# Performance work log

Hardware: AMD Instinct MI355X
Metric: run time of the kernel (lower is better)

Reference implementation:

```python
import jax, jax.numpy as jnp
import numpy as np

N_NODES = 100000
N_EDGES = 1600000
F_IN = 128
D = 2           # stalk dimension (2D rotations)
H = 16          # hidden channels per stalk dim
GH = 64         # gnn hidden of sheaf learner
N_LAYERS = 2
OUT = 10


def setup_inputs() -> dict:
    key = jax.random.key(0)
    ks = jax.random.split(key, 16)
    def w(k, shape):
        fan_in = shape[-2] if len(shape) >= 2 else shape[-1]
        return jax.random.normal(k, shape, dtype=jnp.float32) / jnp.sqrt(jnp.float32(fan_in))
    return {
        "x": jax.random.normal(ks[0], (N_NODES, F_IN), dtype=jnp.float32),
        "edge_index": jax.random.randint(ks[1], (2, N_EDGES), 0, N_NODES, dtype=jnp.int64),
        "W_in": w(ks[2], (F_IN, D * H)),
        "b_in": jnp.zeros((D * H,), jnp.float32),
        "emb1_W": w(ks[3], (D * H, GH)),
        "emb1_b": jnp.zeros((GH,), jnp.float32),
        "Ws1": w(ks[4], (GH, GH)),
        "Wn1": w(ks[5], (GH, GH)),
        "Ws2": w(ks[6], (GH, GH)),
        "Wn2": w(ks[7], (GH, GH)),
        "emb2_W": w(ks[8], (GH, 1)),
        "emb2_b": jnp.zeros((1,), jnp.float32),
        "W_diff": w(ks[9], (N_LAYERS, H, H)),
        "W_out": w(ks[10], (D * H, OUT)),
        "b_out": jnp.zeros((OUT,), jnp.float32),
    }


def reference(x, edge_index, W_in, b_in, emb1_W, emb1_b, Ws1, Wn1, Ws2, Wn2,
              emb2_W, emb2_b, W_diff, W_out, b_out):
    src, dst = edge_index[0], edge_index[1]
    n = x.shape[0]

    # input embedding to node stalk features
    h = x @ W_in + b_in                               # (N, D*H)

    m = jax.nn.gelu(h @ emb1_W + emb1_b)              # (N, GH)
    def sumgnn(m, Ws, Wn):
        agg = jax.ops.segment_sum(m[src], dst, num_segments=n)
        return jax.nn.gelu(m @ Ws + agg @ Wn)
    m = sumgnn(m, Ws1, Wn1)
    m = sumgnn(m, Ws2, Wn2)
    theta = jnp.tanh(m @ emb2_W + emb2_b)             # (N, 1), sheaf_act='tanh'

    # ---- Orthogonal.get_2d_rotation: angle = theta * 2*pi ----
    ang = theta * (2.0 * jnp.pi)
    sin, cos = jnp.sin(ang), jnp.cos(ang)
    R = jnp.concatenate([cos, -sin, sin, cos], axis=1).reshape(-1, 2, 2)  # (N,2,2)

    # symmetric degree normalization (self-loop +1 avoids div-by-zero)
    deg = jax.ops.segment_sum(jnp.ones((src.shape[0],), jnp.float32), dst,
                              num_segments=n) + 1.0
    norm = jax.lax.rsqrt(deg[src] * deg[dst])         # (E,)

    # per-edge transport map M_e = R_dst^T @ R_src  (E,2,2)
    M = jnp.einsum('eba,ebc->eac', R[dst], R[src])

    xs = h.reshape(n, D, H)                           # (N, d, H)
    for l in range(W_diff.shape[0]):
        msg = jnp.einsum('eab,ebh->eah', M, xs[src]) * norm[:, None, None]
        agg = jax.ops.segment_sum(msg, dst, num_segments=n)
        Lx = xs - agg                                 # sheaf Laplacian applied
        xs = xs - jax.nn.gelu(jnp.einsum('ndh,hk->ndk', Lx, W_diff[l]))

    return xs.reshape(n, D * H) @ W_out + b_out       # (N, OUT)
```

## Files before the change

kernel.cpp:

```cpp
#include <hip/hip_runtime.h>
#include <math.h>


typedef unsigned short bf16_t;

#define NSHARD 256
#define CHUNK 4096
#define UPD_NPB 8
#define GNN_NPB 128

__device__ __forceinline__ float bf2f(bf16_t u) {
    return __uint_as_float(((unsigned int)u) << 16);
}
__device__ __forceinline__ bf16_t f2bf(float f) {
    unsigned int u = __float_as_uint(f);
    unsigned int r = (u + 0x7FFFu + ((u >> 16) & 1u)) >> 16;
    return (bf16_t)r;
}

__device__ __forceinline__ unsigned int pack_half2(float a, float b) {
    _Float16 ha = (_Float16)a;
    _Float16 hb = (_Float16)b;
    unsigned short ua = __builtin_bit_cast(unsigned short, ha);
    unsigned short ub = __builtin_bit_cast(unsigned short, hb);
    return (unsigned int)ua | ((unsigned int)ub << 16);
}
__device__ __forceinline__ float2 unpack_half2(unsigned int u) {
    _Float16 lo = __builtin_bit_cast(_Float16, (unsigned short)(u & 0xFFFFu));
    _Float16 hi = __builtin_bit_cast(_Float16, (unsigned short)(u >> 16));
    return make_float2((float)lo, (float)hi);
}

__device__ __forceinline__ float gelu_tanh(float x) {
    float x3 = x * x * x;
    float t = tanhf(0.7978845608028654f * (x + 0.044715f * x3));
    return 0.5f * x * (1.0f + t);
}

__global__ void k_detect(const int* __restrict__ ei, int* __restrict__ flag) {
    if (blockIdx.x == 0 && threadIdx.x == 0) {
        int is64 = 1;
        for (int i = 1; i < 256; i += 2)
            if (ei[i] != 0) { is64 = 0; break; }
        *flag = is64;
    }
}

__global__ __launch_bounds__(256) void k_count(const int* __restrict__ ei,
                        const int* __restrict__ flag, int* __restrict__ shard_cnt,
                        int e, int sn) {
    __shared__ int lc[NSHARD];
    if (threadIdx.x < NSHARD) lc[threadIdx.x] = 0;
    __syncthreads();
    int is64 = *flag;
    int beg = blockIdx.x * CHUNK;
    int end = min(beg + CHUNK, e);
    for (int i = beg + threadIdx.x; i < end; i += 256) {
        int d = is64 ? ei[2 * (e + i)] : ei[e + i];
        atomicAdd(&lc[d / sn], 1);
    }
    __syncthreads();
    if (threadIdx.x < NSHARD) {
        int c = lc[threadIdx.x];
        if (c) atomicAdd(&shard_cnt[threadIdx.x], c);
    }
}

__global__ void k_scan_shard(const int* __restrict__ shard_cnt,
                             int* __restrict__ shard_base, int* __restrict__ bcur) {
    __shared__ int s[NSHARD];
    int t = threadIdx.x;
    s[t] = shard_cnt[t];
    __syncthreads();
#pragma unroll
    for (int off = 1; off < NSHARD; off <<= 1) {
        int add = (t >= off) ? s[t - off] : 0;
        __syncthreads();
        s[t] += add;
        __syncthreads();
    }
    int excl = (t == 0) ? 0 : s[t - 1];
    shard_base[t] = excl;
    bcur[t] = excl;
    if (t == NSHARD - 1) shard_base[NSHARD] = s[t];
}

__global__ __launch_bounds__(256) void k_partition(const int* __restrict__ ei,
                        const int* __restrict__ flag, int* __restrict__ bcur,
                        int2* __restrict__ ebuf, int e, int sn) {
    __shared__ int lcnt[NSHARD];
    __shared__ int lbase[NSHARD];
    int is64 = *flag;
    int beg = blockIdx.x * CHUNK;
    int end = min(beg + CHUNK, e);
    if (threadIdx.x < NSHARD) lcnt[threadIdx.x] = 0;
    __syncthreads();
    for (int i = beg + threadIdx.x; i < end; i += 256) {
        int d = is64 ? ei[2 * (e + i)] : ei[e + i];
        atomicAdd(&lcnt[d / sn], 1);
    }
    __syncthreads();
    if (threadIdx.x < NSHARD) {
        int c = lcnt[threadIdx.x];
        lbase[threadIdx.x] = (c > 0) ? atomicAdd(&bcur[threadIdx.x], c) : 0;
        lcnt[threadIdx.x] = 0;
    }
    __syncthreads();
    for (int i = beg + threadIdx.x; i < end; i += 256) {
        int d = is64 ? ei[2 * (e + i)] : ei[e + i];
        int s = is64 ? ei[2 * i] : ei[i];
        int sh = d / sn;
        int pos = lbase[sh] + atomicAdd(&lcnt[sh], 1);
        ebuf[pos] = make_int2(s, d);
    }
}

__global__ __launch_bounds__(256) void k_distribute(const int* __restrict__ shard_base,
                        const int2* __restrict__ ebuf, int* __restrict__ csr_src,
                        int* __restrict__ row_ptr, int sn, int n) {
    __shared__ int lcnt[512];
    __shared__ int lcur[512];
    __shared__ int stmp[256];
    int sh = blockIdx.x;
    int node0 = sh * sn;
    if (node0 >= n) return;
    int nloc = min(sn, n - node0);
    int base = shard_base[sh];
    int bend = shard_base[sh + 1];
    for (int j = threadIdx.x; j < nloc; j += 256) lcnt[j] = 0;
    __syncthreads();
    for (int p = base + threadIdx.x; p < bend; p += 256) {
        int2 ed = ebuf[p];
        atomicAdd(&lcnt[ed.y - node0], 1);
    }
    __syncthreads();
    int carry = 0;
    for (int seg = 0; seg < nloc; seg += 256) {
        int idx = seg + threadIdx.x;
        int v = (idx < nloc) ? lcnt[idx] : 0;
        stmp[threadIdx.x] = v;
        __syncthreads();
#pragma unroll
        for (int off = 1; off < 256; off <<= 1) {
            int add = (threadIdx.x >= off) ? stmp[threadIdx.x - off] : 0;
            __syncthreads();
            stmp[threadIdx.x] += add;
            __syncthreads();
        }
        int incl = stmp[threadIdx.x];
        if (idx < nloc) {
            lcur[idx] = base + carry + incl - v;
            row_ptr[node0 + idx + 1] = base + carry + incl;
        }
        carry += stmp[255];
        __syncthreads();
    }
    if (sh == 0 && threadIdx.x == 0) row_ptr[0] = 0;
    __syncthreads();
    for (int p = base + threadIdx.x; p < bend; p += 256) {
        int2 ed = ebuf[p];
        int pos = atomicAdd(&lcur[ed.y - node0], 1);
        csr_src[pos] = ed.x;
    }
}

__global__ __launch_bounds__(256) void k_embed_hm(const float* __restrict__ x,
                          const float* __restrict__ W_in, const float* __restrict__ b_in,
                          const float* __restrict__ W2, const float* __restrict__ b2,
                          float* __restrict__ h,
                          unsigned int* __restrict__ m16, int n) {
    __shared__ float sW[128 * 32];
    __shared__ float sX[128 * 68];
    __shared__ float sb1[32];
    __shared__ float sb2[64];
    int tid = threadIdx.x;
    for (int i = tid; i < 128 * 32; i += 256) sW[i] = W_in[i];
    for (int i = tid; i < 32; i += 256) sb1[i] = b_in[i];
    for (int i = tid; i < 64; i += 256) sb2[i] = b2[i];

    int node0 = blockIdx.x * 64;
    {
        int r = tid >> 2;
        int q0 = tid & 3;
        int node_r = node0 + r;
        const float4* xrow = (const float4*)(x + (size_t)node_r * 128);
#pragma unroll
        for (int qq = 0; qq < 8; qq++) {
            int q = qq * 4 + q0;
            float4 v = (node_r < n) ? xrow[q] : make_float4(0.f, 0.f, 0.f, 0.f);
            sX[(q * 4 + 0) * 68 + r] = v.x;
            sX[(q * 4 + 1) * 68 + r] = v.y;
            sX[(q * 4 + 2) * 68 + r] = v.z;
            sX[(q * 4 + 3) * 68 + r] = v.w;
        }
    }
    __syncthreads();

    int tx = tid & 7;
    int ty = tid >> 3;
    float acc[2][4];
#pragma unroll
    for (int i = 0; i < 2; i++)
#pragma unroll
        for (int j = 0; j < 4; j++) acc[i][j] = 0.0f;

#pragma unroll 4
    for (int k = 0; k < 128; k++) {
        float a0 = sX[k * 68 + ty * 2];
        float a1 = sX[k * 68 + ty * 2 + 1];
        float4 wv = *(const float4*)&sW[k * 32 + tx * 4];
#pragma unroll
        for (int j = 0; j < 4; j++) {
            float w = (&wv.x)[j];
            acc[0][j] += a0 * w;
            acc[1][j] += a1 * w;
        }
    }
    __syncthreads();

    float hv[2][4];
#pragma unroll
    for (int i = 0; i < 2; i++) {
        int node = node0 + ty * 2 + i;
#pragma unroll
        for (int j = 0; j < 4; j++) {
            hv[i][j] = acc[i][j] + sb1[tx * 4 + j];
            sX[(tx * 4 + j) * 68 + (ty * 2 + i)] = hv[i][j];
        }
        if (node < n) {
            float4 o = make_float4(hv[i][0], hv[i][1], hv[i][2], hv[i][3]);
            *(float4*)&h[(size_t)node * 32 + tx * 4] = o;
        }
    }
    for (int i = tid; i < 32 * 64; i += 256) sW[i] = W2[i];
    __syncthreads();

    int tx2 = tid & 15;
    int ty2 = tid >> 4;
    float acc2[4][4];
#pragma unroll
    for (int i = 0; i < 4; i++)
#pragma unroll
        for (int j = 0; j < 4; j++) acc2[i][j] = 0.0f;

#pragma unroll 4
    for (int k = 0; k < 32; k++) {
        float4 av = *(const float4*)&sX[k * 68 + ty2 * 4];
        float4 wv = *(const float4*)&sW[k * 64 + tx2 * 4];
        float a_[4] = {av.x, av.y, av.z, av.w};
#pragma unroll
        for (int i = 0; i < 4; i++)
#pragma unroll
            for (int j = 0; j < 4; j++)
                acc2[i][j] += a_[i] * (&wv.x)[j];
    }
#pragma unroll
    for (int i = 0; i < 4; i++) {
        int node = node0 + ty2 * 4 + i;
        if (node >= n) continue;
        float o0 = gelu_tanh(acc2[i][0] + sb2[tx2 * 4]);
        float o1 = gelu_tanh(acc2[i][1] + sb2[tx2 * 4 + 1]);
        float o2 = gelu_tanh(acc2[i][2] + sb2[tx2 * 4 + 2]);
        float o3 = gelu_tanh(acc2[i][3] + sb2[tx2 * 4 + 3]);
        *(uint2*)&m16[(size_t)node * 32 + tx2 * 2] =
            make_uint2(pack_half2(o0, o1), pack_half2(o2, o3));
    }
}

__global__ void k_gather64h(const int* __restrict__ row_ptr, const int* __restrict__ csr_src,
                            const uint2* __restrict__ m16v,
                            unsigned int* __restrict__ agg16, int n) {
    int wave = (blockIdx.x * blockDim.x + threadIdx.x) >> 6;
    int lane = threadIdx.x & 63;
    int f = lane & 15;
    int q = lane >> 4;
    if (wave >= n) return;
    int beg = row_ptr[wave], end = row_ptr[wave + 1];
    float a0 = 0.f, a1 = 0.f, a2 = 0.f, a3 = 0.f;
    int p = beg + q;
    for (; p + 4 < end; p += 8) {
        int s0 = csr_src[p], s1 = csr_src[p + 4];
        uint2 u = m16v[(size_t)s0 * 16 + f];
        uint2 v = m16v[(size_t)s1 * 16 + f];
        float2 ux = unpack_half2(u.x), uy = unpack_half2(u.y);
        float2 vx = unpack_half2(v.x), vy = unpack_half2(v.y);
        a0 += ux.x + vx.x; a1 += ux.y + vx.y;
        a2 += uy.x + vy.x; a3 += uy.y + vy.y;
    }
    if (p < end) {
        uint2 u = m16v[(size_t)csr_src[p] * 16 + f];
        float2 ux = unpack_half2(u.x), uy = unpack_half2(u.y);
        a0 += ux.x; a1 += ux.y; a2 += uy.x; a3 += uy.y;
    }
    a0 += __shfl_xor(a0, 16, 64); a0 += __shfl_xor(a0, 32, 64);
    a1 += __shfl_xor(a1, 16, 64); a1 += __shfl_xor(a1, 32, 64);
    a2 += __shfl_xor(a2, 16, 64); a2 += __shfl_xor(a2, 32, 64);
    a3 += __shfl_xor(a3, 16, 64); a3 += __shfl_xor(a3, 32, 64);
    if (q == 0)
        *(uint2*)&agg16[(size_t)wave * 32 + 2 * f] =
            make_uint2(pack_half2(a0, a1), pack_half2(a2, a3));
}

__global__ __launch_bounds__(128) void k_gnn(
        const unsigned int* A0, const unsigned int* __restrict__ A1,
        const float* __restrict__ Ws, const float* __restrict__ Wn,
        unsigned int* m16out,
        const float* w2, const float* b2, const int* __restrict__ row_ptr,
        const float* __restrict__ xs, float4* __restrict__ params,
        bf16_t* __restrict__ ysh, int n) {
    __shared__ unsigned int sA[32 * 132];
    __shared__ float sW[64 * 64];
    __shared__ float sTh[GNN_NPB];
    int tid = threadIdx.x;
    int tx = tid & 7;
    int ty = tid >> 3;
    int node0 = blockIdx.x * GNN_NPB;
    int nodeBase = node0 + ty * 8;

    float acc[8][8];
#pragma unroll
    for (int i = 0; i < 8; i++)
#pragma unroll
        for (int j = 0; j < 8; j++) acc[i][j] = 0.0f;

#pragma unroll
    for (int phase = 0; phase < 2; phase++) {
        const unsigned int* A = phase ? A1 : A0;
        const float* Wg = phase ? Wn : Ws;
        __syncthreads();
        {
            float4* d = (float4*)sW;
            const float4* s = (const float4*)Wg;
#pragma unroll
            for (int i = 0; i < 8; i++) d[tid + 128 * i] = s[tid + 128 * i];
        }
#pragma unroll
        for (int t = 0; t < 8; t++) {
            int i = tid + 128 * t;
            int nl = i >> 3, p = i & 7;
            int node = node0 + nl;
            uint4 v = make_uint4(0u, 0u, 0u, 0u);
            if (node < n) v = *(const uint4*)&A[(size_t)node * 32 + p * 4];
            int kp = 4 * p;
            sA[(kp + 0) * 132 + nl] = v.x;
            sA[(kp + 1) * 132 + nl] = v.y;
            sA[(kp + 2) * 132 + nl] = v.z;
            sA[(kp + 3) * 132 + nl] = v.w;
        }
        __syncthreads();
#pragma unroll 4
        for (int kp = 0; kp < 32; kp++) {
            uint4 a0 = *(const uint4*)&sA[kp * 132 + ty * 8];
            uint4 a1 = *(const uint4*)&sA[kp * 132 + ty * 8 + 4];
            const float* wr0 = &sW[(2 * kp) * 64 + tx * 8];
            const float* wr1 = &sW[(2 * kp + 1) * 64 + tx * 8];
            float4 wl0 = *(const float4*)wr0;
            float4 wl1 = *(const float4*)(wr0 + 4);
            float4 wh0 = *(const float4*)wr1;
            float4 wh1 = *(const float4*)(wr1 + 4);
            float wlo[8] = {wl0.x, wl0.y, wl0.z, wl0.w, wl1.x, wl1.y, wl1.z, wl1.w};
            float whi[8] = {wh0.x, wh0.y, wh0.z, wh0.w, wh1.x, wh1.y, wh1.z, wh1.w};
            unsigned int au[8] = {a0.x, a0.y, a0.z, a0.w, a1.x, a1.y, a1.z, a1.w};
#pragma unroll
            for (int i = 0; i < 8; i++) {
                float2 a = unpack_half2(au[i]);
#pragma unroll
                for (int j = 0; j < 8; j++)
                    acc[i][j] += a.x * wlo[j] + a.y * whi[j];
            }
        }
    }

    if (m16out) {
#pragma unroll
        for (int i = 0; i < 8; i++) {
            int node = nodeBase + i;
            if (node >= n) continue;
            float o[8];
#pragma unroll
            for (int j = 0; j < 8; j++) o[j] = gelu_tanh(acc[i][j]);
            uint4 pv = make_uint4(pack_half2(o[0], o[1]), pack_half2(o[2], o[3]),
                                  pack_half2(o[4], o[5]), pack_half2(o[6], o[7]));
            *(uint4*)&m16out[(size_t)node * 32 + tx * 4] = pv;
        }
        return;
    }

    float4 w2a = *(const float4*)&w2[tx * 8];
    float4 w2b = *(const float4*)&w2[tx * 8 + 4];
    float part[8];
#pragma unroll
    for (int i = 0; i < 8; i++) {
        float o[8];
#pragma unroll
        for (int j = 0; j < 8; j++) o[j] = gelu_tanh(acc[i][j]);
        part[i] = o[0] * w2a.x + o[1] * w2a.y + o[2] * w2a.z + o[3] * w2a.w +
                  o[4] * w2b.x + o[5] * w2b.y + o[6] * w2b.z + o[7] * w2b.w;
    }
#pragma unroll
    for (int d = 1; d < 8; d <<= 1)
#pragma unroll
        for (int i = 0; i < 8; i++) part[i] += __shfl_xor(part[i], d, 64);
    if (tx == 0) {
#pragma unroll
        for (int i = 0; i < 8; i++) sTh[ty * 8 + i] = part[i];
    }
    __syncthreads();

    {
        int node = node0 + tid;
        if (node < n) {
            float theta = tanhf(sTh[tid] + b2[0]);
            float ang = 6.283185307179586f * theta;
            float cv = cosf(ang), sv = sinf(ang);
            float deg = (float)(row_ptr[node + 1] - row_ptr[node]);
            float rd = rsqrtf(deg + 1.0f);
            params[node] = make_float4(cv, sv, rd, 0.0f);
            const float4* xr = (const float4*)(xs + (size_t)node * 32);
            ushort4* yr = (ushort4*)(ysh + (size_t)node * 32);
#pragma unroll
            for (int q = 0; q < 4; q++) {
                float4 x0 = xr[q];
                float4 x1 = xr[q + 4];
                float x0_[4] = {x0.x, x0.y, x0.z, x0.w};
                float x1_[4] = {x1.x, x1.y, x1.z, x1.w};
                float y0[4], y1[4];
#pragma unroll
                for (int t2 = 0; t2 < 4; t2++) {
                    y0[t2] = rd * (cv * x0_[t2] - sv * x1_[t2]);
                    y1[t2] = rd * (sv * x0_[t2] + cv * x1_[t2]);
                }
                yr[q]     = make_ushort4(f2bf(y0[0]), f2bf(y0[1]), f2bf(y0[2]), f2bf(y0[3]));
                yr[q + 4] = make_ushort4(f2bf(y1[0]), f2bf(y1[1]), f2bf(y1[2]), f2bf(y1[3]));
            }
        }
    }
}

__global__ void k_gather32(const int* __restrict__ row_ptr, const int* __restrict__ csr_src,
                           const uint2* __restrict__ yshv, float* __restrict__ S, int n) {
    int wave = (blockIdx.x * blockDim.x + threadIdx.x) >> 6;
    int lane = threadIdx.x & 63;
    int f = lane & 7;
    int o = lane >> 3;
    if (wave >= n) return;
    int beg = row_ptr[wave], end = row_ptr[wave + 1];
    float a0 = 0.f, a1 = 0.f, a2 = 0.f, a3 = 0.f;
    int p = beg + o;
    for (; p + 8 < end; p += 16) {
        int s0 = csr_src[p], s1 = csr_src[p + 8];
        uint2 u = yshv[(size_t)s0 * 8 + f];
        uint2 v = yshv[(size_t)s1 * 8 + f];
        a0 += __uint_as_float(u.x << 16) + __uint_as_float(v.x << 16);
        a1 += __uint_as_float(u.x & 0xFFFF0000u) + __uint_as_float(v.x & 0xFFFF0000u);
        a2 += __uint_as_float(u.y << 16) + __uint_as_float(v.y << 16);
        a3 += __uint_as_float(u.y & 0xFFFF0000u) + __uint_as_float(v.y & 0xFFFF0000u);
    }
    if (p < end) {
        uint2 u = yshv[(size_t)csr_src[p] * 8 + f];
        a0 += __uint_as_float(u.x << 16);
        a1 += __uint_as_float(u.x & 0xFFFF0000u);
        a2 += __uint_as_float(u.y << 16);
        a3 += __uint_as_float(u.y & 0xFFFF0000u);
    }
    a0 += __shfl_xor(a0, 8, 64); a0 += __shfl_xor(a0, 16, 64); a0 += __shfl_xor(a0, 32, 64);
    a1 += __shfl_xor(a1, 8, 64); a1 += __shfl_xor(a1, 16, 64); a1 += __shfl_xor(a1, 32, 64);
    a2 += __shfl_xor(a2, 8, 64); a2 += __shfl_xor(a2, 16, 64); a2 += __shfl_xor(a2, 32, 64);
    a3 += __shfl_xor(a3, 8, 64); a3 += __shfl_xor(a3, 16, 64); a3 += __shfl_xor(a3, 32, 64);
    if (o == 0)
        *(float4*)&S[(size_t)wave * 32 + 4 * f] = make_float4(a0, a1, a2, a3);
}


__global__ __launch_bounds__(256) void k_update_mid(
                             float* __restrict__ xs, const float* __restrict__ S,
                             const float4* __restrict__ params, const float* __restrict__ Wd,
                             bf16_t* __restrict__ ysh, int n) {
    __shared__ float sWd[256];
    __shared__ __align__(16) float sLx[UPD_NPB][36];
    int tid = threadIdx.x;
    sWd[tid] = Wd[tid];
    int nl = tid >> 5;
    int c  = tid & 31;
    int h  = c & 15;
    int node = blockIdx.x * UPD_NPB + nl;
    bool ok = node < n;
    float4 pd = ok ? params[node] : make_float4(0.f, 0.f, 0.f, 0.f);
    float cd = pd.x, sd = pd.y, rd = pd.z;
    float sv = ok ? S[(size_t)node * 32 + c] : 0.0f;
    float xv = ok ? xs[(size_t)node * 32 + c] : 0.0f;
    float sp = __shfl_xor(sv, 16);
    float sgnA = (c < 16) ? sd : -sd;
    float a = rd * (cd * sv + sgnA * sp);
    sLx[nl][c] = xv - a;
    __syncthreads();
    float wc[16];
#pragma unroll
    for (int k = 0; k < 16; k++) wc[k] = sWd[k * 16 + h];
    const float* lrow = &sLx[nl][c & 16];
    float4 l0 = *(const float4*)(lrow);
    float4 l1 = *(const float4*)(lrow + 4);
    float4 l2 = *(const float4*)(lrow + 8);
    float4 l3 = *(const float4*)(lrow + 12);
    float lv[16] = {l0.x, l0.y, l0.z, l0.w, l1.x, l1.y, l1.z, l1.w,
                    l2.x, l2.y, l2.z, l2.w, l3.x, l3.y, l3.z, l3.w};
    float acc = 0.0f;
#pragma unroll
    for (int k = 0; k < 16; k++) acc += lv[k] * wc[k];
    float nx = xv - gelu_tanh(acc);
    float np = __shfl_xor(nx, 16);
    float sgnY = (c < 16) ? -sd : sd;
    float y = rd * (cd * nx + sgnY * np);
    if (ok) {
        xs[(size_t)node * 32 + c] = nx;
        ysh[(size_t)node * 32 + c] = f2bf(y);
    }
}

__global__ __launch_bounds__(256) void k_update_out(
                             const float* __restrict__ xs, const float* __restrict__ S,
                             const float4* __restrict__ params, const float* __restrict__ Wd,
                             const float* __restrict__ Wo, const float* __restrict__ bo,
                             float* __restrict__ out, int n) {
    __shared__ float sWd[256];
    __shared__ float sWo[320];
    __shared__ float sbo[16];
    __shared__ __align__(16) float sLx[UPD_NPB][36];
    __shared__ float sNx[UPD_NPB][36];
    int tid = threadIdx.x;
    sWd[tid] = Wd[tid];
    for (int i = tid; i < 320; i += 256) sWo[i] = Wo[i];
    if (tid < 10) sbo[tid] = bo[tid];
    int nl = tid >> 5;
    int c  = tid & 31;
    int h  = c & 15;
    int node = blockIdx.x * UPD_NPB + nl;
    bool ok = node < n;
    float4 pd = ok ? params[node] : make_float4(0.f, 0.f, 0.f, 0.f);
    float cd = pd.x, sd = pd.y, rd = pd.z;
    float sv = ok ? S[(size_t)node * 32 + c] : 0.0f;
    float xv = ok ? xs[(size_t)node * 32 + c] : 0.0f;
    float sp = __shfl_xor(sv, 16);
    float sgnA = (c < 16) ? sd : -sd;
    float a = rd * (cd * sv + sgnA * sp);
    sLx[nl][c] = xv - a;
    __syncthreads();
    float wc[16];
#pragma unroll
    for (int k = 0; k < 16; k++) wc[k] = sWd[k * 16 + h];
    const float* lrow = &sLx[nl][c & 16];
    float4 l0 = *(const float4*)(lrow);
    float4 l1 = *(const float4*)(lrow + 4);
    float4 l2 = *(const float4*)(lrow + 8);
    float4 l3 = *(const float4*)(lrow + 12);
    float lv[16] = {l0.x, l0.y, l0.z, l0.w, l1.x, l1.y, l1.z, l1.w,
                    l2.x, l2.y, l2.z, l2.w, l3.x, l3.y, l3.z, l3.w};
    float acc = 0.0f;
#pragma unroll
    for (int k = 0; k < 16; k++) acc += lv[k] * wc[k];
    float nx = xv - gelu_tanh(acc);
    sNx[nl][c] = nx;
    __syncthreads();
    if (tid < UPD_NPB * 10) {
        int nl2 = tid / 10;
        int j = tid - nl2 * 10;
        int node2 = blockIdx.x * UPD_NPB + nl2;
        if (node2 < n) {
            float acc2 = sbo[j];
#pragma unroll 8
            for (int k = 0; k < 32; k++) acc2 += sNx[nl2][k] * sWo[k * 10 + j];
            out[(size_t)node2 * 10 + j] = acc2;
        }
    }
}

static inline size_t align256(size_t x) { return (x + 255) & ~(size_t)255; }

extern "C" void kernel_launch(void* const* d_in, const int* in_sizes, int n_in,
                              void* d_out, int out_size, void* d_ws, size_t ws_size,
                              hipStream_t stream) {
    const float* x      = (const float*)d_in[0];
    const int*   ei     = (const int*)d_in[1];
    const float* W_in   = (const float*)d_in[2];
    const float* b_in   = (const float*)d_in[3];
    const float* emb1_W = (const float*)d_in[4];
    const float* emb1_b = (const float*)d_in[5];
    const float* Ws1    = (const float*)d_in[6];
    const float* Wn1    = (const float*)d_in[7];
    const float* Ws2    = (const float*)d_in[8];
    const float* Wn2    = (const float*)d_in[9];
    const float* emb2_W = (const float*)d_in[10];
    const float* emb2_b = (const float*)d_in[11];
    const float* W_diff = (const float*)d_in[12];
    const float* W_out  = (const float*)d_in[13];
    const float* b_out  = (const float*)d_in[14];

    int n = in_sizes[0] / 128;
    int e = in_sizes[1] / 2;
    int sn = (n + NSHARD - 1) / NSHARD;

    char* base = (char*)d_ws;
    size_t off = 0;
    int*    csr_src   = (int*)(base + off);    off = align256(off + (size_t)e * 4);
    int2*   ebuf      = (int2*)(base + off);   off = align256(off + (size_t)e * 8);
    int*    row_ptr   = (int*)(base + off);    off = align256(off + (size_t)(n + 1) * 4);
    int*    shard_cnt = (int*)(base + off);    off = align256(off + NSHARD * 4);
    int*    shard_base= (int*)(base + off);    off = align256(off + (NSHARD + 1) * 4);
    int*    bcur      = (int*)(base + off);    off = align256(off + NSHARD * 4);
    int*    flag      = (int*)(base + off);    off = align256(off + 16);
    float*  h         = (float*)(base + off);  off = align256(off + (size_t)n * 32 * 4);
    bf16_t* ysh       = (bf16_t*)(base + off); off = align256(off + (size_t)n * 32 * 2);
    float*  agg       = (float*)(base + off);  off = align256(off + (size_t)n * 64 * 4);
    float4* params    = (float4*)(base + off); off = align256(off + (size_t)n * 16);

    unsigned int* m16;
    if ((size_t)n * 64 * 2 <= (size_t)e * 8) {
        m16 = (unsigned int*)ebuf;
    } else {
        m16 = (unsigned int*)(base + off);
        off = align256(off + (size_t)n * 64 * 2);
    }
    unsigned int* agg16 = (unsigned int*)agg;

    int tb64 = (n + 63) / 64;
    int pb = (e + CHUNK - 1) / CHUNK;
    int ub = (n + UPD_NPB - 1) / UPD_NPB;
    int gnnb = (n + GNN_NPB - 1) / GNN_NPB;

    k_detect<<<1, 64, 0, stream>>>(ei, flag);
    hipMemsetAsync(shard_cnt, 0, NSHARD * 4, stream);
    k_count<<<pb, 256, 0, stream>>>(ei, flag, shard_cnt, e, sn);
    k_scan_shard<<<1, NSHARD, 0, stream>>>(shard_cnt, shard_base, bcur);
    k_partition<<<pb, 256, 0, stream>>>(ei, flag, bcur, ebuf, e, sn);
    k_distribute<<<NSHARD, 256, 0, stream>>>(shard_base, ebuf, csr_src, row_ptr, sn, n);

    k_embed_hm<<<tb64, 256, 0, stream>>>(x, W_in, b_in, emb1_W, emb1_b, h, m16, n);

    int gb64 = (n * 64 + 255) / 256;
    k_gather64h<<<gb64, 256, 0, stream>>>(row_ptr, csr_src, (const uint2*)m16, agg16, n);
    k_gnn<<<gnnb, 128, 0, stream>>>(m16, agg16, Ws1, Wn1, m16,
                                    nullptr, nullptr, nullptr, nullptr, nullptr, nullptr, n);
    k_gather64h<<<gb64, 256, 0, stream>>>(row_ptr, csr_src, (const uint2*)m16, agg16, n);
    k_gnn<<<gnnb, 128, 0, stream>>>(m16, agg16, Ws2, Wn2, nullptr,
                                    emb2_W, emb2_b, row_ptr, h, params, ysh, n);

    k_gather32<<<gb64, 256, 0, stream>>>(row_ptr, csr_src, (const uint2*)ysh, agg, n);
    k_update_mid<<<ub, 256, 0, stream>>>(h, agg, params, W_diff, ysh, n);
    k_gather32<<<gb64, 256, 0, stream>>>(row_ptr, csr_src, (const uint2*)ysh, agg, n);
    k_update_out<<<ub, 256, 0, stream>>>(h, agg, params, W_diff + 256,
                                         W_out, b_out, (float*)d_out, n);
}
```

Before: 502.4 us.

## Use fp16 MFMA with split-precision weights for SumGNN dense layers

Replaces the scalar FMA tiled GEMM in the SumGNN layers with MFMA 16x16x32 f16 instructions. A new prep kernel pre-swizzles Ws/Wn into per-lane B fragments, splitting each weight into a high fp16 part and a scaled residual to keep near-fp32 weight precision. A fragments are loaded straight from global memory with no shared-memory staging, and the theta reduction is done with shuffles within 16-lane groups. The cost is two MFMAs per k-block, an extra small launch, and fp16 output stores of 2 bytes per lane that are not coalesced into wide vectors.

```diff
diff --git a/kernel.cpp b/kernel.cpp
--- a/kernel.cpp
+++ b/kernel.cpp
@@ -3,11 +3,13 @@
 
 
 typedef unsigned short bf16_t;
+typedef unsigned int u32x4 __attribute__((ext_vector_type(4)));
+typedef _Float16 half8 __attribute__((ext_vector_type(8)));
+typedef float f32x4 __attribute__((ext_vector_type(4)));
 
 #define NSHARD 256
 #define CHUNK 4096
 #define UPD_NPB 8
-#define GNN_NPB 128
 
 __device__ __forceinline__ float bf2f(bf16_t u) {
     return __uint_as_float(((unsigned int)u) << 16);
@@ -301,114 +303,121 @@
             make_uint2(pack_half2(a0, a1), pack_half2(a2, a3));
 }
 
-__global__ __launch_bounds__(128) void k_gnn(
+__global__ __launch_bounds__(256) void k_prep_bfrag(
+        const float* __restrict__ Ws1, const float* __restrict__ Wn1,
+        const float* __restrict__ Ws2, const float* __restrict__ Wn2,
+        u32x4* __restrict__ bfrag) {
+    int tid = threadIdx.x;
+    for (int it = 0; it < 16; it++) {
+        int idx = it * 256 + tid;
+        int layer = idx >> 11;
+        int hiLo  = (idx >> 10) & 1;
+        int kb    = (idx >> 8) & 3;
+        int ct    = (idx >> 6) & 3;
+        int lane  = idx & 63;
+        int col   = ct * 16 + (lane & 15);
+        int kbase = kb * 32 + (lane >> 4) * 8;
+        const float* Ws = layer ? Ws2 : Ws1;
+        const float* Wn = layer ? Wn2 : Wn1;
+        unsigned int hw[4];
+#pragma unroll
+        for (int jp = 0; jp < 4; jp++) {
+            unsigned short hs[2];
+#pragma unroll
+            for (int t2 = 0; t2 < 2; t2++) {
+                int k = kbase + jp * 2 + t2;
+                float wv = (k < 64) ? Ws[k * 64 + col] : Wn[(k - 64) * 64 + col];
+                _Float16 hi = (_Float16)wv;
+                _Float16 ov = hiLo ? (_Float16)((wv - (float)hi) * 2048.0f) : hi;
+                hs[t2] = __builtin_bit_cast(unsigned short, ov);
+            }
+            hw[jp] = (unsigned int)hs[0] | ((unsigned int)hs[1] << 16);
+        }
+        u32x4 v;
+        v[0] = hw[0]; v[1] = hw[1]; v[2] = hw[2]; v[3] = hw[3];
+        bfrag[idx] = v;
+    }
+}
+
+__global__ __launch_bounds__(256) void k_gnn_mfma(
         const unsigned int* A0, const unsigned int* __restrict__ A1,
-        const float* __restrict__ Ws, const float* __restrict__ Wn,
+        const u32x4* __restrict__ bfrag, int layer,
         unsigned int* m16out,
         const float* w2, const float* b2, const int* __restrict__ row_ptr,
         const float* __restrict__ xs, float4* __restrict__ params,
         bf16_t* __restrict__ ysh, int n) {
-    __shared__ unsigned int sA[32 * 132];
-    __shared__ float sW[64 * 64];
-    __shared__ float sTh[GNN_NPB];
+    __shared__ float sTh[64];
     int tid = threadIdx.x;
-    int tx = tid & 7;
-    int ty = tid >> 3;
-    int node0 = blockIdx.x * GNN_NPB;
-    int nodeBase = node0 + ty * 8;
-
-    float acc[8][8];
-#pragma unroll
-    for (int i = 0; i < 8; i++)
-#pragma unroll
-        for (int j = 0; j < 8; j++) acc[i][j] = 0.0f;
-
-#pragma unroll
-    for (int phase = 0; phase < 2; phase++) {
-        const unsigned int* A = phase ? A1 : A0;
-        const float* Wg = phase ? Wn : Ws;
-        __syncthreads();
-        {
-            float4* d = (float4*)sW;
-            const float4* s = (const float4*)Wg;
-#pragma unroll
-            for (int i = 0; i < 8; i++) d[tid + 128 * i] = s[tid + 128 * i];
-        }
-#pragma unroll
-        for (int t = 0; t < 8; t++) {
-            int i = tid + 128 * t;
-            int nl = i >> 3, p = i & 7;
-            int node = node0 + nl;
-            uint4 v = make_uint4(0u, 0u, 0u, 0u);
-            if (node < n) v = *(const uint4*)&A[(size_t)node * 32 + p * 4];
-            int kp = 4 * p;
-            sA[(kp + 0) * 132 + nl] = v.x;
-            sA[(kp + 1) * 132 + nl] = v.y;
-            sA[(kp + 2) * 132 + nl] = v.z;
-            sA[(kp + 3) * 132 + nl] = v.w;
-        }
-        __syncthreads();
-#pragma unroll 4
-        for (int kp = 0; kp < 32; kp++) {
-            uint4 a0 = *(const uint4*)&sA[kp * 132 + ty * 8];
-            uint4 a1 = *(const uint4*)&sA[kp * 132 + ty * 8 + 4];
-            const float* wr0 = &sW[(2 * kp) * 64 + tx * 8];
-            const float* wr1 = &sW[(2 * kp + 1) * 64 + tx * 8];
-            float4 wl0 = *(const float4*)wr0;
-            float4 wl1 = *(const float4*)(wr0 + 4);
-            float4 wh0 = *(const float4*)wr1;
-            float4 wh1 = *(const float4*)(wr1 + 4);
-            float wlo[8] = {wl0.x, wl0.y, wl0.z, wl0.w, wl1.x, wl1.y, wl1.z, wl1.w};
-            float whi[8] = {wh0.x, wh0.y, wh0.z, wh0.w, wh1.x, wh1.y, wh1.z, wh1.w};
-            unsigned int au[8] = {a0.x, a0.y, a0.z, a0.w, a1.x, a1.y, a1.z, a1.w};
-#pragma unroll
-            for (int i = 0; i < 8; i++) {
-                float2 a = unpack_half2(au[i]);
-#pragma unroll
-                for (int j = 0; j < 8; j++)
-                    acc[i][j] += a.x * wlo[j] + a.y * whi[j];
+    int w = tid >> 6, lane = tid & 63;
+    int g = lane >> 4, c15 = lane & 15;
+    int nodeBase = blockIdx.x * 64 + w * 16;
+
+    int arow = nodeBase + c15;
+    if (arow >= n) arow = n - 1;
+    const u32x4* am = (const u32x4*)(A0 + (size_t)arow * 32);
+    const u32x4* aa = (const u32x4*)(A1 + (size_t)arow * 32);
+    u32x4 afr[4];
+    afr[0] = am[g];
+    afr[1] = am[4 + g];
+    afr[2] = aa[g];
+    afr[3] = aa[4 + g];
+
+    const u32x4* bf = bfrag + layer * 2048;
+    float o[4][4];
+#pragma unroll
+    for (int ct = 0; ct < 4; ct++) {
+        f32x4 ah = {0.f, 0.f, 0.f, 0.f};
+        f32x4 al = {0.f, 0.f, 0.f, 0.f};
+#pragma unroll
+        for (int kb = 0; kb < 4; kb++) {
+            half8 a  = __builtin_bit_cast(half8, afr[kb]);
+            half8 bh = __builtin_bit_cast(half8, bf[(kb << 8) + (ct << 6) + lane]);
+            half8 bl = __builtin_bit_cast(half8, bf[1024 + (kb << 8) + (ct << 6) + lane]);
+            ah = __builtin_amdgcn_mfma_f32_16x16x32_f16(a, bh, ah, 0, 0, 0);
+            al = __builtin_amdgcn_mfma_f32_16x16x32_f16(a, bl, al, 0, 0, 0);
+        }
+#pragma unroll
+        for (int r = 0; r < 4; r++)
+            o[ct][r] = gelu_tanh(ah[r] + al[r] * (1.0f / 2048.0f));
+    }
+
+    if (m16out) {
+        unsigned short* mo = (unsigned short*)m16out;
+#pragma unroll
+        for (int r = 0; r < 4; r++) {
+            int node = nodeBase + g * 4 + r;
+            if (node >= n) continue;
+#pragma unroll
+            for (int ct = 0; ct < 4; ct++) {
+                _Float16 hv = (_Float16)o[ct][r];
+                mo[(size_t)node * 64 + ct * 16 + c15] =
+                    __builtin_bit_cast(unsigned short, hv);
             }
         }
-    }
-
-    if (m16out) {
-#pragma unroll
-        for (int i = 0; i < 8; i++) {
-            int node = nodeBase + i;
-            if (node >= n) continue;
-            float o[8];
-#pragma unroll
-            for (int j = 0; j < 8; j++) o[j] = gelu_tanh(acc[i][j]);
-            uint4 pv = make_uint4(pack_half2(o[0], o[1]), pack_half2(o[2], o[3]),
-                                  pack_half2(o[4], o[5]), pack_half2(o[6], o[7]));
-            *(uint4*)&m16out[(size_t)node * 32 + tx * 4] = pv;
-        }
         return;
     }
 
-    float4 w2a = *(const float4*)&w2[tx * 8];
-    float4 w2b = *(const float4*)&w2[tx * 8 + 4];
-    float part[8];
-#pragma unroll
-    for (int i = 0; i < 8; i++) {
-        float o[8];
-#pragma unroll
-        for (int j = 0; j < 8; j++) o[j] = gelu_tanh(acc[i][j]);
-        part[i] = o[0] * w2a.x + o[1] * w2a.y + o[2] * w2a.z + o[3] * w2a.w +
-                  o[4] * w2b.x + o[5] * w2b.y + o[6] * w2b.z + o[7] * w2b.w;
-    }
-#pragma unroll
-    for (int d = 1; d < 8; d <<= 1)
-#pragma unroll
-        for (int i = 0; i < 8; i++) part[i] += __shfl_xor(part[i], d, 64);
-    if (tx == 0) {
-#pragma unroll
-        for (int i = 0; i < 8; i++) sTh[ty * 8 + i] = part[i];
-    }
-    __syncthreads();
-
     {
-        int node = node0 + tid;
+        float w2v[4];
+#pragma unroll
+        for (int ct = 0; ct < 4; ct++) w2v[ct] = w2[ct * 16 + c15];
+        float part[4];
+#pragma unroll
+        for (int r = 0; r < 4; r++)
+            part[r] = o[0][r] * w2v[0] + o[1][r] * w2v[1] +
+                      o[2][r] * w2v[2] + o[3][r] * w2v[3];
+#pragma unroll
+        for (int d = 1; d < 16; d <<= 1)
+#pragma unroll
+            for (int r = 0; r < 4; r++) part[r] += __shfl_xor(part[r], d, 64);
+        if (c15 == 0) {
+#pragma unroll
+            for (int r = 0; r < 4; r++) sTh[w * 16 + g * 4 + r] = part[r];
+        }
+    }
+    __syncthreads();
+    if (tid < 64) {
+        int node = blockIdx.x * 64 + tid;
         if (node < n) {
             float theta = tanhf(sTh[tid] + b2[0]);
             float ang = 6.283185307179586f * theta;
@@ -612,20 +621,21 @@
     bf16_t* ysh       = (bf16_t*)(base + off); off = align256(off + (size_t)n * 32 * 2);
     float*  agg       = (float*)(base + off);  off = align256(off + (size_t)n * 64 * 4);
     float4* params    = (float4*)(base + off); off = align256(off + (size_t)n * 16);
+    u32x4*  bfrag     = (u32x4*)(base + off);  off = align256(off + 4096 * 16);
 
     unsigned int* m16;
-    if ((size_t)n * 64 * 2 <= (size_t)e * 8) {
+    if ((size_t)n * 64 * 2 + 4096 <= (size_t)e * 8) {
         m16 = (unsigned int*)ebuf;
     } else {
         m16 = (unsigned int*)(base + off);
-        off = align256(off + (size_t)n * 64 * 2);
+        off = align256(off + (size_t)n * 64 * 2 + 4096);
     }
     unsigned int* agg16 = (unsigned int*)agg;
 
     int tb64 = (n + 63) / 64;
     int pb = (e + CHUNK - 1) / CHUNK;
     int ub = (n + UPD_NPB - 1) / UPD_NPB;
-    int gnnb = (n + GNN_NPB - 1) / GNN_NPB;
+    int gnnm = (n + 63) / 64;
 
     k_detect<<<1, 64, 0, stream>>>(ei, flag);
     hipMemsetAsync(shard_cnt, 0, NSHARD * 4, stream);
@@ -634,15 +644,17 @@
     k_partition<<<pb, 256, 0, stream>>>(ei, flag, bcur, ebuf, e, sn);
     k_distribute<<<NSHARD, 256, 0, stream>>>(shard_base, ebuf, csr_src, row_ptr, sn, n);
 
+    k_prep_bfrag<<<1, 256, 0, stream>>>(Ws1, Wn1, Ws2, Wn2, bfrag);
+
     k_embed_hm<<<tb64, 256, 0, stream>>>(x, W_in, b_in, emb1_W, emb1_b, h, m16, n);
 
     int gb64 = (n * 64 + 255) / 256;
     k_gather64h<<<gb64, 256, 0, stream>>>(row_ptr, csr_src, (const uint2*)m16, agg16, n);
-    k_gnn<<<gnnb, 128, 0, stream>>>(m16, agg16, Ws1, Wn1, m16,
-                                    nullptr, nullptr, nullptr, nullptr, nullptr, nullptr, n);
+    k_gnn_mfma<<<gnnm, 256, 0, stream>>>(m16, agg16, bfrag, 0, m16,
+                                         nullptr, nullptr, nullptr, nullptr, nullptr, nullptr, n);
     k_gather64h<<<gb64, 256, 0, stream>>>(row_ptr, csr_src, (const uint2*)m16, agg16, n);
-    k_gnn<<<gnnb, 128, 0, stream>>>(m16, agg16, Ws2, Wn2, nullptr,
-                                    emb2_W, emb2_b, row_ptr, h, params, ysh, n);
+    k_gnn_mfma<<<gnnm, 256, 0, stream>>>(m16, agg16, bfrag, 1, nullptr,
+                                         emb2_W, emb2_b, row_ptr, h, params, ysh, n);
 
     k_gather32<<<gb64, 256, 0, stream>>>(row_ptr, csr_src, (const uint2*)ysh, agg, n);
     k_update_mid<<<ub, 256, 0, stream>>>(h, agg, params, W_diff, ysh, n);
```

Result: faster. 436.5 us (median of 2 runs) (-13.1%).
